# Performance work log

Measured on AMD Instinct MI355X. Metric: run time of the kernel, lower is better.

Reference implementation:

```python
import jax, jax.numpy as jnp
import numpy as np

B = 16384
IN = 512
H = 512

def setup_inputs() -> dict:
    key = jax.random.key(0)
    ks = jax.random.split(key, 8)
    inp = {
        "x_t": jax.random.normal(ks[0], (B, IN), dtype=jnp.float32),
        "h_t": jax.random.normal(ks[1], (B, H), dtype=jnp.float32),
        "W_ir": jax.random.normal(ks[2], (IN, H), dtype=jnp.float32),
        "W_hr": jax.random.normal(ks[3], (H, H), dtype=jnp.float32),
        "b_r": jnp.zeros((H,), dtype=jnp.float32),
        "W_iz": jax.random.normal(ks[4], (IN, H), dtype=jnp.float32),
        "W_hz": jax.random.normal(ks[5], (H, H), dtype=jnp.float32),
        "b_z": jnp.zeros((H,), dtype=jnp.float32),
        "W_in": jax.random.normal(ks[6], (IN, H), dtype=jnp.float32),
        "W_hn": jax.random.normal(ks[7], (H, H), dtype=jnp.float32),
        "b_n": jnp.zeros((H,), dtype=jnp.float32),
    }
    return inp

def reference(x_t, h_t, W_ir, W_hr, b_r, W_iz, W_hz, b_z, W_in, W_hn, b_n):
    # Fuse the three input-side and three hidden-side GEMMs by concatenating weights.
    Wi = jnp.concatenate([W_ir, W_iz, W_in], axis=1)   # [IN, 3H]
    Wh = jnp.concatenate([W_hr, W_hz, W_hn], axis=1)   # [H, 3H]
    gi = x_t @ Wi                                      # [B, 3H]
    gh = h_t @ Wh                                      # [B, 3H]
    h = b_r.shape[0]
    r_t = jax.nn.sigmoid(gi[:, :h] + gh[:, :h] + b_r)
    z_t = jax.nn.sigmoid(gi[:, h:2*h] + gh[:, h:2*h] + b_z)
    n_t = jnp.tanh(gi[:, 2*h:] + r_t * gh[:, 2*h:] + b_n)
    return (1.0 - z_t) * n_t + z_t * h_t
```

## Files before the change

kernel.cpp:

```cpp
#include <hip/hip_runtime.h>
#include <hip/hip_fp16.h>

typedef _Float16 half8 __attribute__((ext_vector_type(8)));
typedef float floatx4 __attribute__((ext_vector_type(4)));

#define WLO_OFF (6 * 512 * 512)
#define WMAT_STRIDE ((size_t)(8 * 16 * 2048))

__global__ __launch_bounds__(256) void permute_w(
    const float* __restrict__ Wir, const float* __restrict__ Whr,
    const float* __restrict__ Wiz, const float* __restrict__ Whz,
    const float* __restrict__ Win, const float* __restrict__ Whn,
    _Float16* __restrict__ wperm) {
  __shared__ __align__(16) float tile[32 * 68];
  const int b = blockIdx.x;
  const int w = b >> 7;
  const int rem = b & 127;
  const int ki = rem >> 3;
  const int nt = rem & 7;
  const float* W = (w == 0) ? Wir : (w == 1) ? Whr : (w == 2) ? Wiz
                 : (w == 3) ? Whz : (w == 4) ? Win : Whn;
  const int k0 = ki * 32, n0 = nt * 64;
  const int t = threadIdx.x;

  const int kk = t >> 3;
  const int nn = (t & 7) * 8;
  const float* src = W + (k0 + kk) * 512 + n0 + nn;
  float4 f0 = *(const float4*)(src);
  float4 f1 = *(const float4*)(src + 4);
  float* drow = tile + kk * 68 + nn;
  *(float4*)(drow) = f0;
  *(float4*)(drow + 4) = f1;
  __syncthreads();

  const int u = t >> 6, l = t & 63;
  const int nloc = 16 * u + (l & 15);
  const int kbase = 8 * (l >> 4);
  half8 vh, vl;
#pragma unroll
  for (int j = 0; j < 8; ++j) {
    float f = tile[(kbase + j) * 68 + nloc];
    _Float16 hi = (_Float16)f;
    _Float16 lo = (_Float16)(f - (float)hi);
    vh[j] = hi;
    vl[j] = lo;
  }
  const size_t off = ((size_t)((w * 8 + nt) * 16 + ki)) * 2048 + t * 8;
  *(half8*)(wperm + off) = vh;
  *(half8*)(wperm + WLO_OFF + off) = vl;
}

__global__ __launch_bounds__(256, 2) void gru_fused(
    const float* __restrict__ x, const float* __restrict__ h,
    const _Float16* __restrict__ wperm,
    const float* __restrict__ br, const float* __restrict__ bz,
    const float* __restrict__ bn, float* __restrict__ out) {
  __shared__ __align__(16) _Float16 ldsA[2 * 4 * 4096];

  const int t = threadIdx.x;
  const int lane = t & 63;
  const int wv = t >> 6;
  const int wm = wv >> 1;
  const int wn = wv & 1;
  const int bid = blockIdx.x;
  const int nt = bid & 7;
  const int mt = bid >> 3;
  const int m0 = mt * 128;
  const int n0 = nt * 64;
  const _Float16* wlo = wperm + WLO_OFF;

  floatx4 acc_r[4][2] = {};
  floatx4 acc_z[4][2] = {};
  floatx4 acc_in[4][2] = {};
  floatx4 acc_hn[4][2] = {};

  const int c1 = t + 256;
  const int mA0 = 16 * (t >> 6) + (t & 15);
  const int kA0 = 8 * ((t & 63) >> 4);
  const int mA1 = 16 * (c1 >> 6) + (c1 & 15);
  const int kA1 = 8 * ((c1 & 63) >> 4);

  const float* px0 = x + (m0 + mA0) * 512 + kA0;
  const float* px1 = x + (m0 + mA1) * 512 + kA1;
  const float* ph0 = h + (m0 + mA0) * 512 + kA0;
  const float* ph1 = h + (m0 + mA1) * 512 + kA1;

  {
    float v[4][8];
    *(float4*)&v[0][0] = *(const float4*)(px0);
    *(float4*)&v[0][4] = *(const float4*)(px0 + 4);
    *(float4*)&v[1][0] = *(const float4*)(px1);
    *(float4*)&v[1][4] = *(const float4*)(px1 + 4);
    *(float4*)&v[2][0] = *(const float4*)(ph0);
    *(float4*)&v[2][4] = *(const float4*)(ph0 + 4);
    *(float4*)&v[3][0] = *(const float4*)(ph1);
    *(float4*)&v[3][4] = *(const float4*)(ph1 + 4);
#pragma unroll
    for (int g = 0; g < 4; ++g) {
      half8 hi, lo;
#pragma unroll
      for (int j = 0; j < 8; ++j) {
        _Float16 a = (_Float16)v[g][j];
        hi[j] = a;
        lo[j] = (_Float16)(v[g][j] - (float)a);
      }
      const int c = (g & 1) ? c1 : t;
      const int which = (g >> 1) * 2;
      *(half8*)(ldsA + which * 4096 + c * 8) = hi;
      *(half8*)(ldsA + (which + 1) * 4096 + c * 8) = lo;
    }
  }
  __syncthreads();

  for (int kt = 0; kt < 16; ++kt) {
    const int cur = kt & 1;
    const _Float16* A = ldsA + cur * 16384;

    float v[4][8];
    if (kt < 15) {
      const int k0 = (kt + 1) * 32;
      *(float4*)&v[0][0] = *(const float4*)(px0 + k0);
      *(float4*)&v[0][4] = *(const float4*)(px0 + k0 + 4);
      *(float4*)&v[1][0] = *(const float4*)(px1 + k0);
      *(float4*)&v[1][4] = *(const float4*)(px1 + k0 + 4);
      *(float4*)&v[2][0] = *(const float4*)(ph0 + k0);
      *(float4*)&v[2][4] = *(const float4*)(ph0 + k0 + 4);
      *(float4*)&v[3][0] = *(const float4*)(ph1 + k0);
      *(float4*)&v[3][4] = *(const float4*)(ph1 + k0 + 4);
    }

    half8 axh[4], ahh[4];
#pragma unroll
    for (int i = 0; i < 4; ++i) {
      const int ao = ((wm * 4 + i) * 64 + lane) * 8;
      axh[i] = *(const half8*)(A + 0 * 4096 + ao);
      ahh[i] = *(const half8*)(A + 2 * 4096 + ao);
    }

#pragma unroll
    for (int jn = 0; jn < 2; ++jn) {
      const int bo = (wn * 2 + jn) * 512 + lane * 8;
      const size_t tb = ((size_t)(nt * 16 + kt)) * 2048 + bo;
      half8 bh_ir = *(const half8*)(wperm + tb + 0 * WMAT_STRIDE);
      half8 bh_hr = *(const half8*)(wperm + tb + 1 * WMAT_STRIDE);
      half8 bh_iz = *(const half8*)(wperm + tb + 2 * WMAT_STRIDE);
      half8 bh_hz = *(const half8*)(wperm + tb + 3 * WMAT_STRIDE);
      half8 bh_in = *(const half8*)(wperm + tb + 4 * WMAT_STRIDE);
      half8 bh_hn = *(const half8*)(wperm + tb + 5 * WMAT_STRIDE);
      half8 bl_ir = *(const half8*)(wlo + tb + 0 * WMAT_STRIDE);
      half8 bl_hr = *(const half8*)(wlo + tb + 1 * WMAT_STRIDE);
      half8 bl_iz = *(const half8*)(wlo + tb + 2 * WMAT_STRIDE);
      half8 bl_hz = *(const half8*)(wlo + tb + 3 * WMAT_STRIDE);
      half8 bl_in = *(const half8*)(wlo + tb + 4 * WMAT_STRIDE);
      half8 bl_hn = *(const half8*)(wlo + tb + 5 * WMAT_STRIDE);
#pragma unroll
      for (int i = 0; i < 4; ++i) {
        const int ao = ((wm * 4 + i) * 64 + lane) * 8;
        half8 axl = *(const half8*)(A + 1 * 4096 + ao);
        half8 ahl = *(const half8*)(A + 3 * 4096 + ao);
        acc_r[i][jn]  = __builtin_amdgcn_mfma_f32_16x16x32_f16(axh[i], bh_ir, acc_r[i][jn], 0, 0, 0);
        acc_r[i][jn]  = __builtin_amdgcn_mfma_f32_16x16x32_f16(axl,    bh_ir, acc_r[i][jn], 0, 0, 0);
        acc_r[i][jn]  = __builtin_amdgcn_mfma_f32_16x16x32_f16(axh[i], bl_ir, acc_r[i][jn], 0, 0, 0);
        acc_r[i][jn]  = __builtin_amdgcn_mfma_f32_16x16x32_f16(ahh[i], bh_hr, acc_r[i][jn], 0, 0, 0);
        acc_r[i][jn]  = __builtin_amdgcn_mfma_f32_16x16x32_f16(ahl,    bh_hr, acc_r[i][jn], 0, 0, 0);
        acc_r[i][jn]  = __builtin_amdgcn_mfma_f32_16x16x32_f16(ahh[i], bl_hr, acc_r[i][jn], 0, 0, 0);
        acc_z[i][jn]  = __builtin_amdgcn_mfma_f32_16x16x32_f16(axh[i], bh_iz, acc_z[i][jn], 0, 0, 0);
        acc_z[i][jn]  = __builtin_amdgcn_mfma_f32_16x16x32_f16(axl,    bh_iz, acc_z[i][jn], 0, 0, 0);
        acc_z[i][jn]  = __builtin_amdgcn_mfma_f32_16x16x32_f16(axh[i], bl_iz, acc_z[i][jn], 0, 0, 0);
        acc_z[i][jn]  = __builtin_amdgcn_mfma_f32_16x16x32_f16(ahh[i], bh_hz, acc_z[i][jn], 0, 0, 0);
        acc_z[i][jn]  = __builtin_amdgcn_mfma_f32_16x16x32_f16(ahl,    bh_hz, acc_z[i][jn], 0, 0, 0);
        acc_z[i][jn]  = __builtin_amdgcn_mfma_f32_16x16x32_f16(ahh[i], bl_hz, acc_z[i][jn], 0, 0, 0);
        acc_in[i][jn] = __builtin_amdgcn_mfma_f32_16x16x32_f16(axh[i], bh_in, acc_in[i][jn], 0, 0, 0);
        acc_in[i][jn] = __builtin_amdgcn_mfma_f32_16x16x32_f16(axl,    bh_in, acc_in[i][jn], 0, 0, 0);
        acc_in[i][jn] = __builtin_amdgcn_mfma_f32_16x16x32_f16(axh[i], bl_in, acc_in[i][jn], 0, 0, 0);
        acc_hn[i][jn] = __builtin_amdgcn_mfma_f32_16x16x32_f16(ahh[i], bh_hn, acc_hn[i][jn], 0, 0, 0);
        acc_hn[i][jn] = __builtin_amdgcn_mfma_f32_16x16x32_f16(ahl,    bh_hn, acc_hn[i][jn], 0, 0, 0);
        acc_hn[i][jn] = __builtin_amdgcn_mfma_f32_16x16x32_f16(ahh[i], bl_hn, acc_hn[i][jn], 0, 0, 0);
      }
    }

    if (kt < 15) {
      _Float16* base = ldsA + (cur ^ 1) * 16384;
#pragma unroll
      for (int g = 0; g < 4; ++g) {
        half8 hi, lo;
#pragma unroll
        for (int j = 0; j < 8; ++j) {
          _Float16 a = (_Float16)v[g][j];
          hi[j] = a;
          lo[j] = (_Float16)(v[g][j] - (float)a);
        }
        const int c = (g & 1) ? c1 : t;
        const int which = (g >> 1) * 2;
        *(half8*)(base + which * 4096 + c * 8) = hi;
        *(half8*)(base + (which + 1) * 4096 + c * 8) = lo;
      }
    }
    __syncthreads();
  }

  const int quad = lane >> 4;
  const int col = lane & 15;
#pragma unroll
  for (int i = 0; i < 4; ++i) {
    const int mbase = m0 + wm * 64 + i * 16 + quad * 4;
#pragma unroll
    for (int jn = 0; jn < 2; ++jn) {
      const int n = n0 + wn * 32 + jn * 16 + col;
      const float vbr = br[n], vbz = bz[n], vbn = bn[n];
#pragma unroll
      for (int r = 0; r < 4; ++r) {
        const int m = mbase + r;
        const float gr = acc_r[i][jn][r] + vbr;
        const float gz = acc_z[i][jn][r] + vbz;
        const float rg = 1.0f / (1.0f + __expf(-gr));
        const float zg = 1.0f / (1.0f + __expf(-gz));
        const float gn = acc_in[i][jn][r] + rg * acc_hn[i][jn][r] + vbn;
        const float e2 = __expf(2.0f * gn);
        const float ntv = 1.0f - 2.0f / (e2 + 1.0f);
        const float hp = h[m * 512 + n];
        out[m * 512 + n] = (1.0f - zg) * ntv + zg * hp;
      }
    }
  }
}

extern "C" void kernel_launch(void* const* d_in, const int* in_sizes, int n_in,
                              void* d_out, int out_size, void* d_ws, size_t ws_size,
                              hipStream_t stream) {
  const float* x   = (const float*)d_in[0];
  const float* h   = (const float*)d_in[1];
  const float* Wir = (const float*)d_in[2];
  const float* Whr = (const float*)d_in[3];
  const float* br  = (const float*)d_in[4];
  const float* Wiz = (const float*)d_in[5];
  const float* Whz = (const float*)d_in[6];
  const float* bz  = (const float*)d_in[7];
  const float* Win = (const float*)d_in[8];
  const float* Whn = (const float*)d_in[9];
  const float* bn  = (const float*)d_in[10];
  float* out = (float*)d_out;
  _Float16* wperm = (_Float16*)d_ws;

  permute_w<<<768, 256, 0, stream>>>(Wir, Whr, Wiz, Whz, Win, Whn, wperm);
  gru_fused<<<1024, 256, 0, stream>>>(x, h, wperm, br, bz, bn, out);
}
```

Baseline: 301.3 us.

## Halve M tile to 64 rows with one 16-column slice per wave

Shrinks the block tile from 128x64 to 64x64, so each of the four waves owns a 64x16 output slice, and doubles the grid to 2048 blocks. Accumulator count per thread drops by half and LDS use halves, which should relieve register pressure and raise occupancy. It also wraps the MFMA section in s_setprio to favour matrix issue. In exchange each weight fragment is reused across fewer rows, so weight traffic from L2 doubles.

```diff
diff --git a/kernel.cpp b/kernel.cpp
--- a/kernel.cpp
+++ b/kernel.cpp
@@ -55,48 +55,36 @@
     const _Float16* __restrict__ wperm,
     const float* __restrict__ br, const float* __restrict__ bz,
     const float* __restrict__ bn, float* __restrict__ out) {
-  __shared__ __align__(16) _Float16 ldsA[2 * 4 * 4096];
+  __shared__ __align__(16) _Float16 ldsA[2 * 4 * 2048];
 
   const int t = threadIdx.x;
   const int lane = t & 63;
-  const int wv = t >> 6;
-  const int wm = wv >> 1;
-  const int wn = wv & 1;
+  const int wn = t >> 6;
   const int bid = blockIdx.x;
   const int nt = bid & 7;
   const int mt = bid >> 3;
-  const int m0 = mt * 128;
+  const int m0 = mt * 64;
   const int n0 = nt * 64;
   const _Float16* wlo = wperm + WLO_OFF;
 
-  floatx4 acc_r[4][2] = {};
-  floatx4 acc_z[4][2] = {};
-  floatx4 acc_in[4][2] = {};
-  floatx4 acc_hn[4][2] = {};
-
-  const int c1 = t + 256;
-  const int mA0 = 16 * (t >> 6) + (t & 15);
-  const int kA0 = 8 * ((t & 63) >> 4);
-  const int mA1 = 16 * (c1 >> 6) + (c1 & 15);
-  const int kA1 = 8 * ((c1 & 63) >> 4);
-
-  const float* px0 = x + (m0 + mA0) * 512 + kA0;
-  const float* px1 = x + (m0 + mA1) * 512 + kA1;
-  const float* ph0 = h + (m0 + mA0) * 512 + kA0;
-  const float* ph1 = h + (m0 + mA1) * 512 + kA1;
+  floatx4 acc_r[4] = {};
+  floatx4 acc_z[4] = {};
+  floatx4 acc_in[4] = {};
+  floatx4 acc_hn[4] = {};
+
+  const int mA = 16 * (t >> 6) + (t & 15);
+  const int kA = 8 * ((t >> 4) & 3);
+  const float* px = x + (m0 + mA) * 512 + kA;
+  const float* ph = h + (m0 + mA) * 512 + kA;
 
   {
-    float v[4][8];
-    *(float4*)&v[0][0] = *(const float4*)(px0);
-    *(float4*)&v[0][4] = *(const float4*)(px0 + 4);
-    *(float4*)&v[1][0] = *(const float4*)(px1);
-    *(float4*)&v[1][4] = *(const float4*)(px1 + 4);
-    *(float4*)&v[2][0] = *(const float4*)(ph0);
-    *(float4*)&v[2][4] = *(const float4*)(ph0 + 4);
-    *(float4*)&v[3][0] = *(const float4*)(ph1);
-    *(float4*)&v[3][4] = *(const float4*)(ph1 + 4);
-#pragma unroll
-    for (int g = 0; g < 4; ++g) {
+    float v[2][8];
+    *(float4*)&v[0][0] = *(const float4*)(px);
+    *(float4*)&v[0][4] = *(const float4*)(px + 4);
+    *(float4*)&v[1][0] = *(const float4*)(ph);
+    *(float4*)&v[1][4] = *(const float4*)(ph + 4);
+#pragma unroll
+    for (int g = 0; g < 2; ++g) {
       half8 hi, lo;
 #pragma unroll
       for (int j = 0; j < 8; ++j) {
@@ -104,85 +92,77 @@
         hi[j] = a;
         lo[j] = (_Float16)(v[g][j] - (float)a);
       }
-      const int c = (g & 1) ? c1 : t;
-      const int which = (g >> 1) * 2;
-      *(half8*)(ldsA + which * 4096 + c * 8) = hi;
-      *(half8*)(ldsA + (which + 1) * 4096 + c * 8) = lo;
+      *(half8*)(ldsA + (g * 2 + 0) * 2048 + t * 8) = hi;
+      *(half8*)(ldsA + (g * 2 + 1) * 2048 + t * 8) = lo;
     }
   }
   __syncthreads();
 
   for (int kt = 0; kt < 16; ++kt) {
-    const int cur = kt & 1;
-    const _Float16* A = ldsA + cur * 16384;
-
-    float v[4][8];
+    const _Float16* A = ldsA + (kt & 1) * 8192;
+
+    float v[2][8];
     if (kt < 15) {
       const int k0 = (kt + 1) * 32;
-      *(float4*)&v[0][0] = *(const float4*)(px0 + k0);
-      *(float4*)&v[0][4] = *(const float4*)(px0 + k0 + 4);
-      *(float4*)&v[1][0] = *(const float4*)(px1 + k0);
-      *(float4*)&v[1][4] = *(const float4*)(px1 + k0 + 4);
-      *(float4*)&v[2][0] = *(const float4*)(ph0 + k0);
-      *(float4*)&v[2][4] = *(const float4*)(ph0 + k0 + 4);
-      *(float4*)&v[3][0] = *(const float4*)(ph1 + k0);
-      *(float4*)&v[3][4] = *(const float4*)(ph1 + k0 + 4);
-    }
+      *(float4*)&v[0][0] = *(const float4*)(px + k0);
+      *(float4*)&v[0][4] = *(const float4*)(px + k0 + 4);
+      *(float4*)&v[1][0] = *(const float4*)(ph + k0);
+      *(float4*)&v[1][4] = *(const float4*)(ph + k0 + 4);
+    }
+
+    const size_t tb = ((size_t)(nt * 16 + kt)) * 2048 + wn * 512 + lane * 8;
+    half8 bh_ir = *(const half8*)(wperm + tb + 0 * WMAT_STRIDE);
+    half8 bh_hr = *(const half8*)(wperm + tb + 1 * WMAT_STRIDE);
+    half8 bh_iz = *(const half8*)(wperm + tb + 2 * WMAT_STRIDE);
+    half8 bh_hz = *(const half8*)(wperm + tb + 3 * WMAT_STRIDE);
+    half8 bh_in = *(const half8*)(wperm + tb + 4 * WMAT_STRIDE);
+    half8 bh_hn = *(const half8*)(wperm + tb + 5 * WMAT_STRIDE);
+    half8 bl_ir = *(const half8*)(wlo + tb + 0 * WMAT_STRIDE);
+    half8 bl_hr = *(const half8*)(wlo + tb + 1 * WMAT_STRIDE);
+    half8 bl_iz = *(const half8*)(wlo + tb + 2 * WMAT_STRIDE);
+    half8 bl_hz = *(const half8*)(wlo + tb + 3 * WMAT_STRIDE);
+    half8 bl_in = *(const half8*)(wlo + tb + 4 * WMAT_STRIDE);
+    half8 bl_hn = *(const half8*)(wlo + tb + 5 * WMAT_STRIDE);
 
     half8 axh[4], ahh[4];
 #pragma unroll
     for (int i = 0; i < 4; ++i) {
-      const int ao = ((wm * 4 + i) * 64 + lane) * 8;
-      axh[i] = *(const half8*)(A + 0 * 4096 + ao);
-      ahh[i] = *(const half8*)(A + 2 * 4096 + ao);
-    }
-
-#pragma unroll
-    for (int jn = 0; jn < 2; ++jn) {
-      const int bo = (wn * 2 + jn) * 512 + lane * 8;
-      const size_t tb = ((size_t)(nt * 16 + kt)) * 2048 + bo;
-      half8 bh_ir = *(const half8*)(wperm + tb + 0 * WMAT_STRIDE);
-      half8 bh_hr = *(const half8*)(wperm + tb + 1 * WMAT_STRIDE);
-      half8 bh_iz = *(const half8*)(wperm + tb + 2 * WMAT_STRIDE);
-      half8 bh_hz = *(const half8*)(wperm + tb + 3 * WMAT_STRIDE);
-      half8 bh_in = *(const half8*)(wperm + tb + 4 * WMAT_STRIDE);
-      half8 bh_hn = *(const half8*)(wperm + tb + 5 * WMAT_STRIDE);
-      half8 bl_ir = *(const half8*)(wlo + tb + 0 * WMAT_STRIDE);
-      half8 bl_hr = *(const half8*)(wlo + tb + 1 * WMAT_STRIDE);
-      half8 bl_iz = *(const half8*)(wlo + tb + 2 * WMAT_STRIDE);
-      half8 bl_hz = *(const half8*)(wlo + tb + 3 * WMAT_STRIDE);
-      half8 bl_in = *(const half8*)(wlo + tb + 4 * WMAT_STRIDE);
-      half8 bl_hn = *(const half8*)(wlo + tb + 5 * WMAT_STRIDE);
-#pragma unroll
-      for (int i = 0; i < 4; ++i) {
-        const int ao = ((wm * 4 + i) * 64 + lane) * 8;
-        half8 axl = *(const half8*)(A + 1 * 4096 + ao);
-        half8 ahl = *(const half8*)(A + 3 * 4096 + ao);
-        acc_r[i][jn]  = __builtin_amdgcn_mfma_f32_16x16x32_f16(axh[i], bh_ir, acc_r[i][jn], 0, 0, 0);
-        acc_r[i][jn]  = __builtin_amdgcn_mfma_f32_16x16x32_f16(axl,    bh_ir, acc_r[i][jn], 0, 0, 0);
-        acc_r[i][jn]  = __builtin_amdgcn_mfma_f32_16x16x32_f16(axh[i], bl_ir, acc_r[i][jn], 0, 0, 0);
-        acc_r[i][jn]  = __builtin_amdgcn_mfma_f32_16x16x32_f16(ahh[i], bh_hr, acc_r[i][jn], 0, 0, 0);
-        acc_r[i][jn]  = __builtin_amdgcn_mfma_f32_16x16x32_f16(ahl,    bh_hr, acc_r[i][jn], 0, 0, 0);
-        acc_r[i][jn]  = __builtin_amdgcn_mfma_f32_16x16x32_f16(ahh[i], bl_hr, acc_r[i][jn], 0, 0, 0);
-        acc_z[i][jn]  = __builtin_amdgcn_mfma_f32_16x16x32_f16(axh[i], bh_iz, acc_z[i][jn], 0, 0, 0);
-        acc_z[i][jn]  = __builtin_amdgcn_mfma_f32_16x16x32_f16(axl,    bh_iz, acc_z[i][jn], 0, 0, 0);
-        acc_z[i][jn]  = __builtin_amdgcn_mfma_f32_16x16x32_f16(axh[i], bl_iz, acc_z[i][jn], 0, 0, 0);
-        acc_z[i][jn]  = __builtin_amdgcn_mfma_f32_16x16x32_f16(ahh[i], bh_hz, acc_z[i][jn], 0, 0, 0);
-        acc_z[i][jn]  = __builtin_amdgcn_mfma_f32_16x16x32_f16(ahl,    bh_hz, acc_z[i][jn], 0, 0, 0);
-        acc_z[i][jn]  = __builtin_amdgcn_mfma_f32_16x16x32_f16(ahh[i], bl_hz, acc_z[i][jn], 0, 0, 0);
-        acc_in[i][jn] = __builtin_amdgcn_mfma_f32_16x16x32_f16(axh[i], bh_in, acc_in[i][jn], 0, 0, 0);
-        acc_in[i][jn] = __builtin_amdgcn_mfma_f32_16x16x32_f16(axl,    bh_in, acc_in[i][jn], 0, 0, 0);
-        acc_in[i][jn] = __builtin_amdgcn_mfma_f32_16x16x32_f16(axh[i], bl_in, acc_in[i][jn], 0, 0, 0);
-        acc_hn[i][jn] = __builtin_amdgcn_mfma_f32_16x16x32_f16(ahh[i], bh_hn, acc_hn[i][jn], 0, 0, 0);
-        acc_hn[i][jn] = __builtin_amdgcn_mfma_f32_16x16x32_f16(ahl,    bh_hn, acc_hn[i][jn], 0, 0, 0);
-        acc_hn[i][jn] = __builtin_amdgcn_mfma_f32_16x16x32_f16(ahh[i], bl_hn, acc_hn[i][jn], 0, 0, 0);
-      }
-    }
+      const int ao = (i * 64 + lane) * 8;
+      axh[i] = *(const half8*)(A + 0 * 2048 + ao);
+      ahh[i] = *(const half8*)(A + 2 * 2048 + ao);
+    }
+
+    __builtin_amdgcn_s_setprio(1);
+#pragma unroll
+    for (int i = 0; i < 4; ++i) {
+      const int ao = (i * 64 + lane) * 8;
+      half8 axl = *(const half8*)(A + 1 * 2048 + ao);
+      half8 ahl = *(const half8*)(A + 3 * 2048 + ao);
+      acc_r[i]  = __builtin_amdgcn_mfma_f32_16x16x32_f16(axh[i], bh_ir, acc_r[i], 0, 0, 0);
+      acc_r[i]  = __builtin_amdgcn_mfma_f32_16x16x32_f16(axl,    bh_ir, acc_r[i], 0, 0, 0);
+      acc_r[i]  = __builtin_amdgcn_mfma_f32_16x16x32_f16(axh[i], bl_ir, acc_r[i], 0, 0, 0);
+      acc_r[i]  = __builtin_amdgcn_mfma_f32_16x16x32_f16(ahh[i], bh_hr, acc_r[i], 0, 0, 0);
+      acc_r[i]  = __builtin_amdgcn_mfma_f32_16x16x32_f16(ahl,    bh_hr, acc_r[i], 0, 0, 0);
+      acc_r[i]  = __builtin_amdgcn_mfma_f32_16x16x32_f16(ahh[i], bl_hr, acc_r[i], 0, 0, 0);
+      acc_z[i]  = __builtin_amdgcn_mfma_f32_16x16x32_f16(axh[i], bh_iz, acc_z[i], 0, 0, 0);
+      acc_z[i]  = __builtin_amdgcn_mfma_f32_16x16x32_f16(axl,    bh_iz, acc_z[i], 0, 0, 0);
+      acc_z[i]  = __builtin_amdgcn_mfma_f32_16x16x32_f16(axh[i], bl_iz, acc_z[i], 0, 0, 0);
+      acc_z[i]  = __builtin_amdgcn_mfma_f32_16x16x32_f16(ahh[i], bh_hz, acc_z[i], 0, 0, 0);
+      acc_z[i]  = __builtin_amdgcn_mfma_f32_16x16x32_f16(ahl,    bh_hz, acc_z[i], 0, 0, 0);
+      acc_z[i]  = __builtin_amdgcn_mfma_f32_16x16x32_f16(ahh[i], bl_hz, acc_z[i], 0, 0, 0);
+      acc_in[i] = __builtin_amdgcn_mfma_f32_16x16x32_f16(axh[i], bh_in, acc_in[i], 0, 0, 0);
+      acc_in[i] = __builtin_amdgcn_mfma_f32_16x16x32_f16(axl,    bh_in, acc_in[i], 0, 0, 0);
+      acc_in[i] = __builtin_amdgcn_mfma_f32_16x16x32_f16(axh[i], bl_in, acc_in[i], 0, 0, 0);
+      acc_hn[i] = __builtin_amdgcn_mfma_f32_16x16x32_f16(ahh[i], bh_hn, acc_hn[i], 0, 0, 0);
+      acc_hn[i] = __builtin_amdgcn_mfma_f32_16x16x32_f16(ahl,    bh_hn, acc_hn[i], 0, 0, 0);
+      acc_hn[i] = __builtin_amdgcn_mfma_f32_16x16x32_f16(ahh[i], bl_hn, acc_hn[i], 0, 0, 0);
+    }
+    __builtin_amdgcn_s_setprio(0);
 
     if (kt < 15) {
-      _Float16* base = ldsA + (cur ^ 1) * 16384;
-#pragma unroll
-      for (int g = 0; g < 4; ++g) {
+      _Float16* base = ldsA + ((kt & 1) ^ 1) * 8192;
+#pragma unroll
+      for (int g = 0; g < 2; ++g) {
         half8 hi, lo;
 #pragma unroll
         for (int j = 0; j < 8; ++j) {
@@ -190,10 +170,8 @@
           hi[j] = a;
           lo[j] = (_Float16)(v[g][j] - (float)a);
         }
-        const int c = (g & 1) ? c1 : t;
-        const int which = (g >> 1) * 2;
-        *(half8*)(base + which * 4096 + c * 8) = hi;
-        *(half8*)(base + (which + 1) * 4096 + c * 8) = lo;
+        *(half8*)(base + (g * 2 + 0) * 2048 + t * 8) = hi;
+        *(half8*)(base + (g * 2 + 1) * 2048 + t * 8) = lo;
       }
     }
     __syncthreads();
@@ -201,26 +179,23 @@
 
   const int quad = lane >> 4;
   const int col = lane & 15;
+  const int n = n0 + wn * 16 + col;
+  const float vbr = br[n], vbz = bz[n], vbn = bn[n];
 #pragma unroll
   for (int i = 0; i < 4; ++i) {
-    const int mbase = m0 + wm * 64 + i * 16 + quad * 4;
-#pragma unroll
-    for (int jn = 0; jn < 2; ++jn) {
-      const int n = n0 + wn * 32 + jn * 16 + col;
-      const float vbr = br[n], vbz = bz[n], vbn = bn[n];
-#pragma unroll
-      for (int r = 0; r < 4; ++r) {
-        const int m = mbase + r;
-        const float gr = acc_r[i][jn][r] + vbr;
-        const float gz = acc_z[i][jn][r] + vbz;
-        const float rg = 1.0f / (1.0f + __expf(-gr));
-        const float zg = 1.0f / (1.0f + __expf(-gz));
-        const float gn = acc_in[i][jn][r] + rg * acc_hn[i][jn][r] + vbn;
-        const float e2 = __expf(2.0f * gn);
-        const float ntv = 1.0f - 2.0f / (e2 + 1.0f);
-        const float hp = h[m * 512 + n];
-        out[m * 512 + n] = (1.0f - zg) * ntv + zg * hp;
-      }
+    const int mbase = m0 + i * 16 + quad * 4;
+#pragma unroll
+    for (int r = 0; r < 4; ++r) {
+      const int m = mbase + r;
+      const float gr = acc_r[i][r] + vbr;
+      const float gz = acc_z[i][r] + vbz;
+      const float rg = 1.0f / (1.0f + __expf(-gr));
+      const float zg = 1.0f / (1.0f + __expf(-gz));
+      const float gn = acc_in[i][r] + rg * acc_hn[i][r] + vbn;
+      const float e2 = __expf(2.0f * gn);
+      const float ntv = 1.0f - 2.0f / (e2 + 1.0f);
+      const float hp = h[m * 512 + n];
+      out[m * 512 + n] = (1.0f - zg) * ntv + zg * hp;
     }
   }
 }
@@ -243,5 +218,5 @@
   _Float16* wperm = (_Float16*)d_ws;
 
   permute_w<<<768, 256, 0, stream>>>(Wir, Whr, Wiz, Whz, Win, Whn, wperm);
-  gru_fused<<<1024, 256, 0, stream>>>(x, h, wperm, br, bz, bn, out);
+  gru_fused<<<2048, 256, 0, stream>>>(x, h, wperm, br, bz, bn, out);
 }
```

Result: faster. 275.3 us (-8.6%).

## Repartition waves to 128x16 tiles, hoist B loads, add scheduling barriers and priority

Applied to the files above, without the earlier changes.

Each of the four waves now owns all 128 rows and a 16-column strip, where before each wave held a 64x32 sub-tile. Each wave therefore loads its B fragments once per k-step, hoisted to the top of the loop and fenced by sched_barrier. A fragments are now read from LDS for every row block, about twice as many LDS reads per wave, while global B loads per wave are halved. The MFMA chain is reordered to interleave the accumulators to reduce dependency stalls, and s_setprio raises wave priority during the MFMA block.

```diff
diff --git a/kernel.cpp b/kernel.cpp
--- a/kernel.cpp
+++ b/kernel.cpp
@@ -59,9 +59,7 @@
 
   const int t = threadIdx.x;
   const int lane = t & 63;
-  const int wv = t >> 6;
-  const int wm = wv >> 1;
-  const int wn = wv & 1;
+  const int wn = t >> 6;
   const int bid = blockIdx.x;
   const int nt = bid & 7;
   const int mt = bid >> 3;
@@ -69,21 +67,18 @@
   const int n0 = nt * 64;
   const _Float16* wlo = wperm + WLO_OFF;
 
-  floatx4 acc_r[4][2] = {};
-  floatx4 acc_z[4][2] = {};
-  floatx4 acc_in[4][2] = {};
-  floatx4 acc_hn[4][2] = {};
-
-  const int c1 = t + 256;
-  const int mA0 = 16 * (t >> 6) + (t & 15);
-  const int kA0 = 8 * ((t & 63) >> 4);
-  const int mA1 = 16 * (c1 >> 6) + (c1 & 15);
-  const int kA1 = 8 * ((c1 & 63) >> 4);
-
-  const float* px0 = x + (m0 + mA0) * 512 + kA0;
-  const float* px1 = x + (m0 + mA1) * 512 + kA1;
-  const float* ph0 = h + (m0 + mA0) * 512 + kA0;
-  const float* ph1 = h + (m0 + mA1) * 512 + kA1;
+  floatx4 acc_r[8] = {};
+  floatx4 acc_z[8] = {};
+  floatx4 acc_in[8] = {};
+  floatx4 acc_hn[8] = {};
+
+  const int mA = 16 * (t >> 6) + (t & 15);
+  const int kA = 8 * ((t >> 4) & 3);
+  const float* px0 = x + (m0 + mA) * 512 + kA;
+  const float* ph0 = h + (m0 + mA) * 512 + kA;
+  const float* px1 = px0 + 64 * 512;
+  const float* ph1 = ph0 + 64 * 512;
+  const int c0 = t, c1 = t + 256;
 
   {
     float v[4][8];
@@ -104,17 +99,31 @@
         hi[j] = a;
         lo[j] = (_Float16)(v[g][j] - (float)a);
       }
-      const int c = (g & 1) ? c1 : t;
-      const int which = (g >> 1) * 2;
-      *(half8*)(ldsA + which * 4096 + c * 8) = hi;
-      *(half8*)(ldsA + (which + 1) * 4096 + c * 8) = lo;
+      const int c = (g & 1) ? c1 : c0;
+      const int part = (g >> 1) * 2;
+      *(half8*)(ldsA + (part + 0) * 4096 + c * 8) = hi;
+      *(half8*)(ldsA + (part + 1) * 4096 + c * 8) = lo;
     }
   }
   __syncthreads();
 
   for (int kt = 0; kt < 16; ++kt) {
-    const int cur = kt & 1;
-    const _Float16* A = ldsA + cur * 16384;
+    const _Float16* A = ldsA + (kt & 1) * 16384;
+
+    const size_t tb = ((size_t)(nt * 16 + kt)) * 2048 + wn * 512 + lane * 8;
+    half8 bh_ir = *(const half8*)(wperm + tb + 0 * WMAT_STRIDE);
+    half8 bh_hr = *(const half8*)(wperm + tb + 1 * WMAT_STRIDE);
+    half8 bh_iz = *(const half8*)(wperm + tb + 2 * WMAT_STRIDE);
+    half8 bh_hz = *(const half8*)(wperm + tb + 3 * WMAT_STRIDE);
+    half8 bh_in = *(const half8*)(wperm + tb + 4 * WMAT_STRIDE);
+    half8 bh_hn = *(const half8*)(wperm + tb + 5 * WMAT_STRIDE);
+    half8 bl_ir = *(const half8*)(wlo + tb + 0 * WMAT_STRIDE);
+    half8 bl_hr = *(const half8*)(wlo + tb + 1 * WMAT_STRIDE);
+    half8 bl_iz = *(const half8*)(wlo + tb + 2 * WMAT_STRIDE);
+    half8 bl_hz = *(const half8*)(wlo + tb + 3 * WMAT_STRIDE);
+    half8 bl_in = *(const half8*)(wlo + tb + 4 * WMAT_STRIDE);
+    half8 bl_hn = *(const half8*)(wlo + tb + 5 * WMAT_STRIDE);
+    __builtin_amdgcn_sched_barrier(0);
 
     float v[4][8];
     if (kt < 15) {
@@ -128,59 +137,39 @@
       *(float4*)&v[3][0] = *(const float4*)(ph1 + k0);
       *(float4*)&v[3][4] = *(const float4*)(ph1 + k0 + 4);
     }
-
-    half8 axh[4], ahh[4];
-#pragma unroll
-    for (int i = 0; i < 4; ++i) {
-      const int ao = ((wm * 4 + i) * 64 + lane) * 8;
-      axh[i] = *(const half8*)(A + 0 * 4096 + ao);
-      ahh[i] = *(const half8*)(A + 2 * 4096 + ao);
-    }
-
-#pragma unroll
-    for (int jn = 0; jn < 2; ++jn) {
-      const int bo = (wn * 2 + jn) * 512 + lane * 8;
-      const size_t tb = ((size_t)(nt * 16 + kt)) * 2048 + bo;
-      half8 bh_ir = *(const half8*)(wperm + tb + 0 * WMAT_STRIDE);
-      half8 bh_hr = *(const half8*)(wperm + tb + 1 * WMAT_STRIDE);
-      half8 bh_iz = *(const half8*)(wperm + tb + 2 * WMAT_STRIDE);
-      half8 bh_hz = *(const half8*)(wperm + tb + 3 * WMAT_STRIDE);
-      half8 bh_in = *(const half8*)(wperm + tb + 4 * WMAT_STRIDE);
-      half8 bh_hn = *(const half8*)(wperm + tb + 5 * WMAT_STRIDE);
-      half8 bl_ir = *(const half8*)(wlo + tb + 0 * WMAT_STRIDE);
-      half8 bl_hr = *(const half8*)(wlo + tb + 1 * WMAT_STRIDE);
-      half8 bl_iz = *(const half8*)(wlo + tb + 2 * WMAT_STRIDE);
-      half8 bl_hz = *(const half8*)(wlo + tb + 3 * WMAT_STRIDE);
-      half8 bl_in = *(const half8*)(wlo + tb + 4 * WMAT_STRIDE);
-      half8 bl_hn = *(const half8*)(wlo + tb + 5 * WMAT_STRIDE);
-#pragma unroll
-      for (int i = 0; i < 4; ++i) {
-        const int ao = ((wm * 4 + i) * 64 + lane) * 8;
-        half8 axl = *(const half8*)(A + 1 * 4096 + ao);
-        half8 ahl = *(const half8*)(A + 3 * 4096 + ao);
-        acc_r[i][jn]  = __builtin_amdgcn_mfma_f32_16x16x32_f16(axh[i], bh_ir, acc_r[i][jn], 0, 0, 0);
-        acc_r[i][jn]  = __builtin_amdgcn_mfma_f32_16x16x32_f16(axl,    bh_ir, acc_r[i][jn], 0, 0, 0);
-        acc_r[i][jn]  = __builtin_amdgcn_mfma_f32_16x16x32_f16(axh[i], bl_ir, acc_r[i][jn], 0, 0, 0);
-        acc_r[i][jn]  = __builtin_amdgcn_mfma_f32_16x16x32_f16(ahh[i], bh_hr, acc_r[i][jn], 0, 0, 0);
-        acc_r[i][jn]  = __builtin_amdgcn_mfma_f32_16x16x32_f16(ahl,    bh_hr, acc_r[i][jn], 0, 0, 0);
-        acc_r[i][jn]  = __builtin_amdgcn_mfma_f32_16x16x32_f16(ahh[i], bl_hr, acc_r[i][jn], 0, 0, 0);
-        acc_z[i][jn]  = __builtin_amdgcn_mfma_f32_16x16x32_f16(axh[i], bh_iz, acc_z[i][jn], 0, 0, 0);
-        acc_z[i][jn]  = __builtin_amdgcn_mfma_f32_16x16x32_f16(axl,    bh_iz, acc_z[i][jn], 0, 0, 0);
-        acc_z[i][jn]  = __builtin_amdgcn_mfma_f32_16x16x32_f16(axh[i], bl_iz, acc_z[i][jn], 0, 0, 0);
-        acc_z[i][jn]  = __builtin_amdgcn_mfma_f32_16x16x32_f16(ahh[i], bh_hz, acc_z[i][jn], 0, 0, 0);
-        acc_z[i][jn]  = __builtin_amdgcn_mfma_f32_16x16x32_f16(ahl,    bh_hz, acc_z[i][jn], 0, 0, 0);
-        acc_z[i][jn]  = __builtin_amdgcn_mfma_f32_16x16x32_f16(ahh[i], bl_hz, acc_z[i][jn], 0, 0, 0);
-        acc_in[i][jn] = __builtin_amdgcn_mfma_f32_16x16x32_f16(axh[i], bh_in, acc_in[i][jn], 0, 0, 0);
-        acc_in[i][jn] = __builtin_amdgcn_mfma_f32_16x16x32_f16(axl,    bh_in, acc_in[i][jn], 0, 0, 0);
-        acc_in[i][jn] = __builtin_amdgcn_mfma_f32_16x16x32_f16(axh[i], bl_in, acc_in[i][jn], 0, 0, 0);
-        acc_hn[i][jn] = __builtin_amdgcn_mfma_f32_16x16x32_f16(ahh[i], bh_hn, acc_hn[i][jn], 0, 0, 0);
-        acc_hn[i][jn] = __builtin_amdgcn_mfma_f32_16x16x32_f16(ahl,    bh_hn, acc_hn[i][jn], 0, 0, 0);
-        acc_hn[i][jn] = __builtin_amdgcn_mfma_f32_16x16x32_f16(ahh[i], bl_hn, acc_hn[i][jn], 0, 0, 0);
-      }
-    }
+    __builtin_amdgcn_sched_barrier(0);
+
+    __builtin_amdgcn_s_setprio(1);
+#pragma unroll
+    for (int i = 0; i < 8; ++i) {
+      const int ao = (i * 64 + lane) * 8;
+      half8 axh = *(const half8*)(A + 0 * 4096 + ao);
+      half8 axl = *(const half8*)(A + 1 * 4096 + ao);
+      half8 ahh = *(const half8*)(A + 2 * 4096 + ao);
+      half8 ahl = *(const half8*)(A + 3 * 4096 + ao);
+      acc_r[i]  = __builtin_amdgcn_mfma_f32_16x16x32_f16(axh, bh_ir, acc_r[i], 0, 0, 0);
+      acc_r[i]  = __builtin_amdgcn_mfma_f32_16x16x32_f16(ahh, bh_hr, acc_r[i], 0, 0, 0);
+      acc_z[i]  = __builtin_amdgcn_mfma_f32_16x16x32_f16(axh, bh_iz, acc_z[i], 0, 0, 0);
+      acc_z[i]  = __builtin_amdgcn_mfma_f32_16x16x32_f16(ahh, bh_hz, acc_z[i], 0, 0, 0);
+      acc_in[i] = __builtin_amdgcn_mfma_f32_16x16x32_f16(axh, bh_in, acc_in[i], 0, 0, 0);
+      acc_hn[i] = __builtin_amdgcn_mfma_f32_16x16x32_f16(ahh, bh_hn, acc_hn[i], 0, 0, 0);
+      acc_r[i]  = __builtin_amdgcn_mfma_f32_16x16x32_f16(axl, bh_ir, acc_r[i], 0, 0, 0);
+      acc_r[i]  = __builtin_amdgcn_mfma_f32_16x16x32_f16(ahl, bh_hr, acc_r[i], 0, 0, 0);
+      acc_z[i]  = __builtin_amdgcn_mfma_f32_16x16x32_f16(axl, bh_iz, acc_z[i], 0, 0, 0);
+      acc_z[i]  = __builtin_amdgcn_mfma_f32_16x16x32_f16(ahl, bh_hz, acc_z[i], 0, 0, 0);
+      acc_in[i] = __builtin_amdgcn_mfma_f32_16x16x32_f16(axl, bh_in, acc_in[i], 0, 0, 0);
+      acc_hn[i] = __builtin_amdgcn_mfma_f32_16x16x32_f16(ahl, bh_hn, acc_hn[i], 0, 0, 0);
+      acc_r[i]  = __builtin_amdgcn_mfma_f32_16x16x32_f16(axh, bl_ir, acc_r[i], 0, 0, 0);
+      acc_r[i]  = __builtin_amdgcn_mfma_f32_16x16x32_f16(ahh, bl_hr, acc_r[i], 0, 0, 0);
+      acc_z[i]  = __builtin_amdgcn_mfma_f32_16x16x32_f16(axh, bl_iz, acc_z[i], 0, 0, 0);
+      acc_z[i]  = __builtin_amdgcn_mfma_f32_16x16x32_f16(ahh, bl_hz, acc_z[i], 0, 0, 0);
+      acc_in[i] = __builtin_amdgcn_mfma_f32_16x16x32_f16(axh, bl_in, acc_in[i], 0, 0, 0);
+      acc_hn[i] = __builtin_amdgcn_mfma_f32_16x16x32_f16(ahh, bl_hn, acc_hn[i], 0, 0, 0);
+    }
+    __builtin_amdgcn_s_setprio(0);
 
     if (kt < 15) {
-      _Float16* base = ldsA + (cur ^ 1) * 16384;
+      _Float16* base = ldsA + ((kt & 1) ^ 1) * 16384;
 #pragma unroll
       for (int g = 0; g < 4; ++g) {
         half8 hi, lo;
@@ -190,10 +179,10 @@
           hi[j] = a;
           lo[j] = (_Float16)(v[g][j] - (float)a);
         }
-        const int c = (g & 1) ? c1 : t;
-        const int which = (g >> 1) * 2;
-        *(half8*)(base + which * 4096 + c * 8) = hi;
-        *(half8*)(base + (which + 1) * 4096 + c * 8) = lo;
+        const int c = (g & 1) ? c1 : c0;
+        const int part = (g >> 1) * 2;
+        *(half8*)(base + (part + 0) * 4096 + c * 8) = hi;
+        *(half8*)(base + (part + 1) * 4096 + c * 8) = lo;
       }
     }
     __syncthreads();
@@ -201,26 +190,23 @@
 
   const int quad = lane >> 4;
   const int col = lane & 15;
-#pragma unroll
-  for (int i = 0; i < 4; ++i) {
-    const int mbase = m0 + wm * 64 + i * 16 + quad * 4;
-#pragma unroll
-    for (int jn = 0; jn < 2; ++jn) {
-      const int n = n0 + wn * 32 + jn * 16 + col;
-      const float vbr = br[n], vbz = bz[n], vbn = bn[n];
-#pragma unroll
-      for (int r = 0; r < 4; ++r) {
-        const int m = mbase + r;
-        const float gr = acc_r[i][jn][r] + vbr;
-        const float gz = acc_z[i][jn][r] + vbz;
-        const float rg = 1.0f / (1.0f + __expf(-gr));
-        const float zg = 1.0f / (1.0f + __expf(-gz));
-        const float gn = acc_in[i][jn][r] + rg * acc_hn[i][jn][r] + vbn;
-        const float e2 = __expf(2.0f * gn);
-        const float ntv = 1.0f - 2.0f / (e2 + 1.0f);
-        const float hp = h[m * 512 + n];
-        out[m * 512 + n] = (1.0f - zg) * ntv + zg * hp;
-      }
+  const int n = n0 + wn * 16 + col;
+  const float vbr = br[n], vbz = bz[n], vbn = bn[n];
+#pragma unroll
+  for (int i = 0; i < 8; ++i) {
+    const int mbase = m0 + i * 16 + quad * 4;
+#pragma unroll
+    for (int r = 0; r < 4; ++r) {
+      const int m = mbase + r;
+      const float gr = acc_r[i][r] + vbr;
+      const float gz = acc_z[i][r] + vbz;
+      const float rg = 1.0f / (1.0f + __expf(-gr));
+      const float zg = 1.0f / (1.0f + __expf(-gz));
+      const float gn = acc_in[i][r] + rg * acc_hn[i][r] + vbn;
+      const float e2 = __expf(2.0f * gn);
+      const float ntv = 1.0f - 2.0f / (e2 + 1.0f);
+      const float hp = h[m * 512 + n];
+      out[m * 512 + n] = (1.0f - zg) * ntv + zg * hp;
     }
   }
 }
```

New measurement: 251.8 us. -16.4%, faster.
